# Optimization experiments

Measured on AMD Instinct MI355X. Metric: run time of the kernel, lower is better.

The kernel has to match this reference:

```python
import jax, jax.numpy as jnp
import numpy as np

B, S, E, H = 2, 4096, 512, 8
D = E // H  # head_dim = 64


def setup_inputs() -> dict:
    key = jax.random.key(0)
    ks = jax.random.split(key, 5)
    s = E ** -0.5
    return {
        "x": jax.random.normal(ks[0], (B, S, E), dtype=jnp.float32),
        "w_qkv": jax.random.normal(ks[1], (E, 3 * E), dtype=jnp.float32) * s,
        "b_qkv": jnp.zeros((3 * E,), dtype=jnp.float32),
        "w_out": jax.random.normal(ks[2], (E, E), dtype=jnp.float32) * s,
        "b_out": jnp.zeros((E,), dtype=jnp.float32),
    }


def reference(x, w_qkv, b_qkv, w_out, b_out):
    # qkv projection: [B,S,3E] -> [3,B,H,S,D]
    qkv = (x @ w_qkv + b_qkv).reshape(B, S, 3, H, D).transpose(2, 0, 3, 1, 4)
    q, k, v = qkv[0], qkv[1], qkv[2]
    # full score matrix [B,H,S,S] (faithful to the unfused torch impl)
    attn = jnp.einsum("bhqd,bhkd->bhqk", q, k) * (D ** -0.5)
    attn = jax.nn.softmax(attn, axis=-1)
    # dropout in eval mode -> identity (deterministic reference)
    out = jnp.einsum("bhqk,bhkd->bhqd", attn, v)  # [B,H,S,D]
    out = out.transpose(0, 2, 1, 3).reshape(B, S, E)
    return out @ w_out + b_out
```

## Files before the change

### kernel.cpp

```cpp
#include <hip/hip_runtime.h>
#include <hip/hip_bf16.h>

typedef __attribute__((ext_vector_type(8))) short bf16x8;
typedef __attribute__((ext_vector_type(4))) float f32x4;

#define MFMA16 __builtin_amdgcn_mfma_f32_16x16x32_bf16

__device__ __forceinline__ unsigned short f2bf(float f) {
  unsigned int u = __builtin_bit_cast(unsigned int, f);
  u += 0x7FFFu + ((u >> 16) & 1u);
  return (unsigned short)(u >> 16);
}

__device__ __forceinline__ void load_lds16(const void* g, void* l) {
  __builtin_amdgcn_global_load_lds(
      (const __attribute__((address_space(1))) unsigned int*)g,
      (__attribute__((address_space(3))) unsigned int*)l, 16, 0, 0);
}

__global__ __launch_bounds__(256) void prep_kernel(
    const float* __restrict__ x, const float* __restrict__ wqkv,
    const float* __restrict__ wout, unsigned short* __restrict__ xb,
    unsigned short* __restrict__ wqkvT, unsigned short* __restrict__ woutT) {
  int blk = blockIdx.x;
  int t = threadIdx.x;
  if (blk < 4096) {
    int i = (blk * 256 + t) * 4;
    float4 v = *(const float4*)(x + i);
    ushort4 o;
    o.x = f2bf(v.x); o.y = f2bf(v.y); o.z = f2bf(v.z); o.w = f2bf(v.w);
    *(ushort4*)(xb + i) = o;
  } else if (blk < 4864) {
    int u = ((blk - 4096) * 256 + t) * 4;
    int k = u / 1536, n = u % 1536;
    float4 v = *(const float4*)(wqkv + (size_t)k * 1536 + n);
    wqkvT[(size_t)(n + 0) * 512 + k] = f2bf(v.x);
    wqkvT[(size_t)(n + 1) * 512 + k] = f2bf(v.y);
    wqkvT[(size_t)(n + 2) * 512 + k] = f2bf(v.z);
    wqkvT[(size_t)(n + 3) * 512 + k] = f2bf(v.w);
  } else {
    int u = ((blk - 4864) * 256 + t) * 4;
    int k = u >> 9, n = u & 511;
    float4 v = *(const float4*)(wout + (size_t)k * 512 + n);
    woutT[(size_t)(n + 0) * 512 + k] = f2bf(v.x);
    woutT[(size_t)(n + 1) * 512 + k] = f2bf(v.y);
    woutT[(size_t)(n + 2) * 512 + k] = f2bf(v.z);
    woutT[(size_t)(n + 3) * 512 + k] = f2bf(v.w);
  }
}

__global__ __launch_bounds__(256, 2) void qkv_gemm(
    const unsigned short* __restrict__ xb, const unsigned short* __restrict__ bt,
    const float* __restrict__ bias, unsigned short* __restrict__ qout,
    unsigned short* __restrict__ ksw, unsigned short* __restrict__ vtsw) {
  __shared__ unsigned short As[128 * 32];
  __shared__ unsigned short Bs[128 * 32];
  const int t = threadIdx.x;
  const int lane = t & 63;
  const int llo = lane & 15, lhi = lane >> 4;
  const int w = t >> 6, wr = w >> 1, wc = w & 1;
  const int m0 = blockIdx.x * 128, n0 = blockIdx.y * 128;

  f32x4 acc[4][4];
#pragma unroll
  for (int i = 0; i < 4; ++i)
#pragma unroll
    for (int j = 0; j < 4; ++j) acc[i][j] = (f32x4){0.f, 0.f, 0.f, 0.f};

  const int r0 = t >> 2;
  const int sb = (t & 3) * 16;

  for (int k0 = 0; k0 < 512; k0 += 32) {
    const char* ga = (const char*)xb + (size_t)(m0 + r0) * 1024 + k0 * 2 + sb;
    const char* gb = (const char*)bt + (size_t)(n0 + r0) * 1024 + k0 * 2 + sb;
    load_lds16(ga, (char*)As + t * 16);
    load_lds16(ga + 64 * 1024, (char*)As + 4096 + t * 16);
    load_lds16(gb, (char*)Bs + t * 16);
    load_lds16(gb + 64 * 1024, (char*)Bs + 4096 + t * 16);
    __syncthreads();

    bf16x8 af[4], bf[4];
#pragma unroll
    for (int mi = 0; mi < 4; ++mi)
      af[mi] = *(const bf16x8*)(As + (wr * 64 + mi * 16 + llo) * 32 + lhi * 8);
#pragma unroll
    for (int ni = 0; ni < 4; ++ni)
      bf[ni] = *(const bf16x8*)(Bs + (wc * 64 + ni * 16 + llo) * 32 + lhi * 8);
#pragma unroll
    for (int mi = 0; mi < 4; ++mi)
#pragma unroll
      for (int ni = 0; ni < 4; ++ni)
        acc[mi][ni] = MFMA16(af[mi], bf[ni], acc[mi][ni], 0, 0, 0);
    __syncthreads();
  }

#pragma unroll
  for (int ni = 0; ni < 4; ++ni) {
    int col = n0 + wc * 64 + ni * 16 + llo;
    float bv = bias[col];
    int sec = col >> 9;
    int h = (col >> 6) & 7;
    int d = col & 63;
#pragma unroll
    for (int mi = 0; mi < 4; ++mi) {
      int rowb = m0 + wr * 64 + mi * 16 + lhi * 4;
#pragma unroll
      for (int r = 0; r < 4; ++r) {
        int m = rowb + r;
        int b = m >> 12, s = m & 4095;
        int bh = (b << 3) + h;
        float val = acc[mi][ni][r] + bv;
        if (sec == 0) {
          qout[((size_t)bh * 4096 + s) * 64 + d] = f2bf(val * 0.18033688f);
        } else if (sec == 1) {
          size_t byte = (size_t)bh * 524288 + (size_t)(s >> 6) * 8192 +
                        (size_t)(s & 63) * 128 + ((d * 2) ^ ((s & 7) << 4));
          *(unsigned short*)((char*)ksw + byte) = f2bf(val);
        } else {
          int u64k = s & 63;
          int c = u64k >> 4, u = u64k & 15;
          int kperm = ((c >> 1) << 5) + ((u >> 2) << 3) + ((c & 1) << 2) + (u & 3);
          size_t byte = (size_t)bh * 524288 + (size_t)(s >> 6) * 8192 +
                        (size_t)d * 128 + ((kperm * 2) ^ ((d & 7) << 4));
          *(unsigned short*)((char*)vtsw + byte) = f2bf(val);
        }
      }
    }
  }
}

__global__ __launch_bounds__(256, 2) void attn_kernel(
    const unsigned short* __restrict__ qp, const unsigned short* __restrict__ ksw,
    const unsigned short* __restrict__ vtsw, unsigned short* __restrict__ aout) {
  __shared__ unsigned short Ks[2][4096];
  __shared__ unsigned short Vts[2][4096];

  const int t = threadIdx.x, lane = t & 63, w = t >> 6;
  const int llo = lane & 15, lhi = lane >> 4;

  const int wg = blockIdx.x + (blockIdx.y << 5);
  const int pidx = ((wg & 7) << 6) + (wg >> 3);
  const int bh = pidx >> 5;
  const int q0 = (pidx & 31) * 128 + w * 32;

  bf16x8 qf[2][2];
#pragma unroll
  for (int qs = 0; qs < 2; ++qs)
#pragma unroll
    for (int f = 0; f < 2; ++f) {
      int row = q0 + qs * 16 + llo;
      int d = f * 32 + lhi * 8;
      qf[qs][f] = *(const bf16x8*)(qp + ((size_t)bh * 4096 + row) * 64 + d);
    }

  float lpart[2] = {0.f, 0.f};
  f32x4 o[2][4];
#pragma unroll
  for (int qs = 0; qs < 2; ++qs)
#pragma unroll
    for (int di = 0; di < 4; ++di) o[qs][di] = (f32x4){0.f, 0.f, 0.f, 0.f};

  const char* kbase = (const char*)ksw + (size_t)bh * 524288;
  const char* vbase = (const char*)vtsw + (size_t)bh * 524288;

  bf16x8 pf[2][2];

  auto stage_tile = [&](const char* g, char* d) {
    load_lds16(g + t * 16, d + t * 16);
    load_lds16(g + 4096 + t * 16, d + 4096 + t * 16);
  };

  auto qkt = [&](f32x4 (&sc)[2][4], const char* kbuf) {
    __builtin_amdgcn_s_setprio(1);
#pragma unroll
    for (int c = 0; c < 4; ++c) {
      int krow = c * 16 + llo;
      int sw = (krow & 7) << 4;
      bf16x8 kf0 = *(const bf16x8*)(kbuf + krow * 128 + ((lhi * 16) ^ sw));
      bf16x8 kf1 = *(const bf16x8*)(kbuf + krow * 128 + ((lhi * 16 + 64) ^ sw));
#pragma unroll
      for (int qs = 0; qs < 2; ++qs) {
        sc[qs][c] = MFMA16(kf0, qf[qs][0], (f32x4){0.f, 0.f, 0.f, 0.f}, 0, 0, 0);
        sc[qs][c] = MFMA16(kf1, qf[qs][1], sc[qs][c], 0, 0, 0);
      }
    }
    __builtin_amdgcn_s_setprio(0);
  };

  auto softmax_pack = [&](f32x4 (&sc)[2][4]) {
#pragma unroll
    for (int qs = 0; qs < 2; ++qs) {
      float e[4][4];
#pragma unroll
      for (int c = 0; c < 4; ++c)
#pragma unroll
        for (int r = 0; r < 4; ++r) {
          e[c][r] = __builtin_amdgcn_exp2f(sc[qs][c][r]);
          lpart[qs] += e[c][r];
        }
#pragma unroll
      for (int f = 0; f < 2; ++f) {
        bf16x8 pvv;
#pragma unroll
        for (int j = 0; j < 8; ++j)
          pvv[j] = __builtin_bit_cast(short,
                       __float2bfloat16(e[2 * f + (j >> 2)][j & 3]));
        pf[qs][f] = pvv;
      }
    }
  };

  auto pv_accum = [&](const char* vbuf) {
    __builtin_amdgcn_s_setprio(1);
#pragma unroll
    for (int f = 0; f < 2; ++f)
#pragma unroll
      for (int di = 0; di < 4; ++di) {
        int vrow = di * 16 + llo;
        int byte = vrow * 128 + ((lhi * 16 + f * 64) ^ ((vrow & 7) << 4));
        bf16x8 vf = *(const bf16x8*)(vbuf + byte);
#pragma unroll
        for (int qs = 0; qs < 2; ++qs)
          o[qs][di] = MFMA16(pf[qs][f], vf, o[qs][di], 0, 0, 0);
      }
    __builtin_amdgcn_s_setprio(0);
  };

  stage_tile(kbase, (char*)&Ks[0][0]);
  stage_tile(vbase, (char*)&Vts[0][0]);
  stage_tile(kbase + 8192, (char*)&Ks[1][0]);
  __syncthreads();

  f32x4 scA[2][4], scB[2][4];
  qkt(scA, (const char*)&Ks[0][0]);
  __syncthreads();

  for (int kt = 0; kt < 62; kt += 2) {
    stage_tile(kbase + (size_t)(kt + 2) * 8192, (char*)&Ks[0][0]);
    stage_tile(vbase + (size_t)(kt + 1) * 8192, (char*)&Vts[1][0]);
    qkt(scB, (const char*)&Ks[1][0]);
    softmax_pack(scA);
    pv_accum((const char*)&Vts[0][0]);
    __syncthreads();
    stage_tile(kbase + (size_t)(kt + 3) * 8192, (char*)&Ks[1][0]);
    stage_tile(vbase + (size_t)(kt + 2) * 8192, (char*)&Vts[0][0]);
    qkt(scA, (const char*)&Ks[0][0]);
    softmax_pack(scB);
    pv_accum((const char*)&Vts[1][0]);
    __syncthreads();
  }

  stage_tile(vbase + (size_t)63 * 8192, (char*)&Vts[1][0]);
  qkt(scB, (const char*)&Ks[1][0]);
  softmax_pack(scA);
  pv_accum((const char*)&Vts[0][0]);
  __syncthreads();
  softmax_pack(scB);
  pv_accum((const char*)&Vts[1][0]);

  float linv[2][4];
#pragma unroll
  for (int qs = 0; qs < 2; ++qs) {
    float s = lpart[qs];
    s += __shfl_xor(s, 16, 64);
    s += __shfl_xor(s, 32, 64);
#pragma unroll
    for (int r = 0; r < 4; ++r)
      linv[qs][r] = 1.f / __shfl(s, lhi * 4 + r, 64);
  }

  int b = bh >> 3, h = bh & 7;
#pragma unroll
  for (int qs = 0; qs < 2; ++qs)
#pragma unroll
    for (int di = 0; di < 4; ++di)
#pragma unroll
      for (int r = 0; r < 4; ++r) {
        int s = q0 + qs * 16 + lhi * 4 + r;
        int d = di * 16 + llo;
        float val = o[qs][di][r] * linv[qs][r];
        aout[((size_t)b * 4096 + s) * 512 + h * 64 + d] = f2bf(val);
      }
}

__global__ __launch_bounds__(256, 2) void out_gemm(
    const unsigned short* __restrict__ ab, const unsigned short* __restrict__ bt,
    const float* __restrict__ bias, float* __restrict__ out) {
  __shared__ unsigned short As[128 * 32];
  __shared__ unsigned short Bs[128 * 32];
  const int t = threadIdx.x;
  const int lane = t & 63;
  const int llo = lane & 15, lhi = lane >> 4;
  const int w = t >> 6, wr = w >> 1, wc = w & 1;
  const int m0 = blockIdx.x * 128, n0 = blockIdx.y * 128;

  f32x4 acc[4][4];
#pragma unroll
  for (int i = 0; i < 4; ++i)
#pragma unroll
    for (int j = 0; j < 4; ++j) acc[i][j] = (f32x4){0.f, 0.f, 0.f, 0.f};

  const int r0 = t >> 2;
  const int sb = (t & 3) * 16;

  for (int k0 = 0; k0 < 512; k0 += 32) {
    const char* ga = (const char*)ab + (size_t)(m0 + r0) * 1024 + k0 * 2 + sb;
    const char* gb = (const char*)bt + (size_t)(n0 + r0) * 1024 + k0 * 2 + sb;
    load_lds16(ga, (char*)As + t * 16);
    load_lds16(ga + 64 * 1024, (char*)As + 4096 + t * 16);
    load_lds16(gb, (char*)Bs + t * 16);
    load_lds16(gb + 64 * 1024, (char*)Bs + 4096 + t * 16);
    __syncthreads();

    bf16x8 af[4], bf[4];
#pragma unroll
    for (int mi = 0; mi < 4; ++mi)
      af[mi] = *(const bf16x8*)(As + (wr * 64 + mi * 16 + llo) * 32 + lhi * 8);
#pragma unroll
    for (int ni = 0; ni < 4; ++ni)
      bf[ni] = *(const bf16x8*)(Bs + (wc * 64 + ni * 16 + llo) * 32 + lhi * 8);
#pragma unroll
    for (int mi = 0; mi < 4; ++mi)
#pragma unroll
      for (int ni = 0; ni < 4; ++ni)
        acc[mi][ni] = MFMA16(af[mi], bf[ni], acc[mi][ni], 0, 0, 0);
    __syncthreads();
  }

#pragma unroll
  for (int ni = 0; ni < 4; ++ni) {
    int col = n0 + wc * 64 + ni * 16 + llo;
    float bv = bias[col];
#pragma unroll
    for (int mi = 0; mi < 4; ++mi) {
      int rowb = m0 + wr * 64 + mi * 16 + lhi * 4;
#pragma unroll
      for (int r = 0; r < 4; ++r)
        out[(size_t)(rowb + r) * 512 + col] = acc[mi][ni][r] + bv;
    }
  }
}

extern "C" void kernel_launch(void* const* d_in, const int* in_sizes, int n_in,
                              void* d_out, int out_size, void* d_ws, size_t ws_size,
                              hipStream_t stream) {
  const float* x = (const float*)d_in[0];
  const float* wqkv = (const float*)d_in[1];
  const float* bqkv = (const float*)d_in[2];
  const float* wout = (const float*)d_in[3];
  const float* bout = (const float*)d_in[4];
  float* out = (float*)d_out;

  char* ws = (char*)d_ws;
  unsigned short* xb    = (unsigned short*)(ws + 0);
  unsigned short* wqkvT = (unsigned short*)(ws + 8388608);
  unsigned short* woutT = (unsigned short*)(ws + 9961472);
  unsigned short* qb    = (unsigned short*)(ws + 10485760);
  unsigned short* ksw   = (unsigned short*)(ws + 18874368);
  unsigned short* vtsw  = (unsigned short*)(ws + 27262976);
  unsigned short* ab    = (unsigned short*)(ws + 35651584);
  (void)ws_size; (void)in_sizes; (void)n_in; (void)out_size;

  prep_kernel<<<5120, 256, 0, stream>>>(x, wqkv, wout, xb, wqkvT, woutT);
  qkv_gemm<<<dim3(64, 12), 256, 0, stream>>>(xb, wqkvT, bqkv, qb, ksw, vtsw);
  attn_kernel<<<dim3(32, 16), 256, 0, stream>>>(qb, ksw, vtsw, ab);
  out_gemm<<<dim3(64, 4), 256, 0, stream>>>(ab, woutT, bout, out);
}
```

Measured before the change: 132.2 us.

## Load V tiles directly from global into registers instead of staging through LDS

The V^T tiles no longer go through shared memory. Each lane now loads its MFMA B-operand fragments straight from global memory into double-buffered registers (vA/vB), and the projection kernel drops the XOR swizzle from the V^T layout. This halves the LDS footprint, which could allow more occupancy, and removes the LDS write and read for V. In exchange it raises register pressure (16 extra bf16x8 registers per lane) and relies on global/L2 latency being hidden by the software pipeline. Each of the four waves fetches the same V data redundantly.

```diff
diff --git a/kernel.cpp b/kernel.cpp
--- a/kernel.cpp
+++ b/kernel.cpp
@@ -121,7 +121,7 @@
           int c = u64k >> 4, u = u64k & 15;
           int kperm = ((c >> 1) << 5) + ((u >> 2) << 3) + ((c & 1) << 2) + (u & 3);
           size_t byte = (size_t)bh * 524288 + (size_t)(s >> 6) * 8192 +
-                        (size_t)d * 128 + ((kperm * 2) ^ ((d & 7) << 4));
+                        (size_t)d * 128 + kperm * 2;
           *(unsigned short*)((char*)vtsw + byte) = f2bf(val);
         }
       }
@@ -133,7 +133,6 @@
     const unsigned short* __restrict__ qp, const unsigned short* __restrict__ ksw,
     const unsigned short* __restrict__ vtsw, unsigned short* __restrict__ aout) {
   __shared__ unsigned short Ks[2][4096];
-  __shared__ unsigned short Vts[2][4096];
 
   const int t = threadIdx.x, lane = t & 63, w = t >> 6;
   const int llo = lane & 15, lhi = lane >> 4;
@@ -162,12 +161,24 @@
 
   const char* kbase = (const char*)ksw + (size_t)bh * 524288;
   const char* vbase = (const char*)vtsw + (size_t)bh * 524288;
+  const char* vlane = vbase + llo * 128 + lhi * 16;
 
   bf16x8 pf[2][2];
-
-  auto stage_tile = [&](const char* g, char* d) {
+  bf16x8 vA[8], vB[8];
+
+  auto stage_k = [&](int kt, char* d) {
+    const char* g = kbase + (size_t)kt * 8192;
     load_lds16(g + t * 16, d + t * 16);
     load_lds16(g + 4096 + t * 16, d + 4096 + t * 16);
+  };
+
+  auto vload = [&](bf16x8 (&vr)[8], int kt) {
+    const char* vt = vlane + (size_t)kt * 8192;
+#pragma unroll
+    for (int f = 0; f < 2; ++f)
+#pragma unroll
+      for (int di = 0; di < 4; ++di)
+        vr[f * 4 + di] = *(const bf16x8*)(vt + di * 2048 + f * 64);
   };
 
   auto qkt = [&](f32x4 (&sc)[2][4], const char* kbuf) {
@@ -210,15 +221,13 @@
     }
   };
 
-  auto pv_accum = [&](const char* vbuf) {
+  auto pv_accum = [&](bf16x8 (&vr)[8]) {
     __builtin_amdgcn_s_setprio(1);
 #pragma unroll
     for (int f = 0; f < 2; ++f)
 #pragma unroll
       for (int di = 0; di < 4; ++di) {
-        int vrow = di * 16 + llo;
-        int byte = vrow * 128 + ((lhi * 16 + f * 64) ^ ((vrow & 7) << 4));
-        bf16x8 vf = *(const bf16x8*)(vbuf + byte);
+        bf16x8 vf = vr[f * 4 + di];
 #pragma unroll
         for (int qs = 0; qs < 2; ++qs)
           o[qs][di] = MFMA16(pf[qs][f], vf, o[qs][di], 0, 0, 0);
@@ -226,9 +235,9 @@
     __builtin_amdgcn_s_setprio(0);
   };
 
-  stage_tile(kbase, (char*)&Ks[0][0]);
-  stage_tile(vbase, (char*)&Vts[0][0]);
-  stage_tile(kbase + 8192, (char*)&Ks[1][0]);
+  stage_k(0, (char*)&Ks[0][0]);
+  stage_k(1, (char*)&Ks[1][0]);
+  vload(vA, 0);
   __syncthreads();
 
   f32x4 scA[2][4], scB[2][4];
@@ -236,27 +245,26 @@
   __syncthreads();
 
   for (int kt = 0; kt < 62; kt += 2) {
-    stage_tile(kbase + (size_t)(kt + 2) * 8192, (char*)&Ks[0][0]);
-    stage_tile(vbase + (size_t)(kt + 1) * 8192, (char*)&Vts[1][0]);
+    stage_k(kt + 2, (char*)&Ks[0][0]);
+    vload(vB, kt + 1);
     qkt(scB, (const char*)&Ks[1][0]);
     softmax_pack(scA);
-    pv_accum((const char*)&Vts[0][0]);
-    __syncthreads();
-    stage_tile(kbase + (size_t)(kt + 3) * 8192, (char*)&Ks[1][0]);
-    stage_tile(vbase + (size_t)(kt + 2) * 8192, (char*)&Vts[0][0]);
+    pv_accum(vA);
+    __syncthreads();
+    stage_k(kt + 3, (char*)&Ks[1][0]);
+    vload(vA, kt + 2);
     qkt(scA, (const char*)&Ks[0][0]);
     softmax_pack(scB);
-    pv_accum((const char*)&Vts[1][0]);
-    __syncthreads();
-  }
-
-  stage_tile(vbase + (size_t)63 * 8192, (char*)&Vts[1][0]);
+    pv_accum(vB);
+    __syncthreads();
+  }
+
+  vload(vB, 63);
   qkt(scB, (const char*)&Ks[1][0]);
   softmax_pack(scA);
-  pv_accum((const char*)&Vts[0][0]);
-  __syncthreads();
+  pv_accum(vA);
   softmax_pack(scB);
-  pv_accum((const char*)&Vts[1][0]);
+  pv_accum(vB);
 
   float linv[2][4];
 #pragma unroll
```

Result: slower. 180.7 us (+36.7%).
